# Performance work log

Measured on AMD Instinct MI355X. Metric: run time of the kernel, lower is better.

## Reference

```python
import jax, jax.numpy as jnp
import numpy as np

N = 100_000   # number of sparse points
C = 128       # channels
K3 = 27       # 3x3x3 kernel offsets


def sparse_conv(x, nbr, W, b):
    """Minkowski-style sparse conv: gather-GEMM-scatter.
    x:   [N, Cin] point features
    nbr: [N, K3] neighbor index per kernel offset; index N -> missing (zero row)
    W:   [K3, Cin, Cout], b: [Cout]
    """
    x_pad = jnp.concatenate([x, jnp.zeros((1, x.shape[1]), x.dtype)], axis=0)

    def step(acc, wk_nk):
        Wk, nk = wk_nk                      # Wk: [Cin,Cout], nk: [N]
        return acc + x_pad[nk] @ Wk, None   # gather + GEMM, accumulate

    acc0 = jnp.broadcast_to(b, (x.shape[0], W.shape[2])).astype(x.dtype)
    acc, _ = jax.lax.scan(step, acc0, (W, nbr.T))
    return acc


def setup_inputs() -> dict:
    key = jax.random.key(0)
    ks = jax.random.split(key, 12)
    Ch = C // 2

    def w(k, shape, fan_in):
        return jax.random.normal(k, shape, dtype=jnp.float32) / np.sqrt(fan_in)

    x = jax.random.normal(ks[0], (N, C), dtype=jnp.float32)
    # neighbor map; value N means "no neighbor" (maps to zero-padded row)
    nbr = jax.random.randint(ks[1], (N, K3), 0, N + 1, dtype=jnp.int32)

    return {
        "x": x,
        "nbr": nbr,
        "W00": w(ks[2], (K3, C, Ch), K3 * C),   # conv0_0: kxkxk, C -> C/2
        "b00": jnp.zeros((Ch,), jnp.float32),
        "W01": w(ks[3], (K3, Ch, Ch), K3 * Ch),  # conv0_1: kxkxk, C/2 -> C/2
        "b01": jnp.zeros((Ch,), jnp.float32),
        "W10": w(ks[4], (C, Ch), C),             # conv1_0: 1x1x1, C -> C/2
        "b10": jnp.zeros((Ch,), jnp.float32),
        "W11": w(ks[5], (K3, Ch, Ch), K3 * Ch),  # conv1_1: kxkxk, C/2 -> C/2
        "b11": jnp.zeros((Ch,), jnp.float32),
        "W12": w(ks[6], (Ch, Ch), Ch),           # conv1_2: 1x1x1, C/2 -> C/2
        "b12": jnp.zeros((Ch,), jnp.float32),
    }


def reference(x, nbr, W00, b00, W01, b01, W10, b10, W11, b11, W12, b12):
    # branch 0: conv -> relu -> conv
    h0 = jax.nn.relu(sparse_conv(x, nbr, W00, b00))
    out0 = sparse_conv(h0, nbr, W01, b01)
    # branch 1: 1x1 conv -> relu -> conv -> relu -> 1x1 conv
    h1 = jax.nn.relu(x @ W10 + b10)
    h1 = jax.nn.relu(sparse_conv(h1, nbr, W11, b11))
    out1 = h1 @ W12 + b12
    # concat channels, residual add
    return jnp.concatenate([out0, out1], axis=1) + x
```

## Files before the change

kernel.cpp:

```cpp
#include <hip/hip_runtime.h>
#include <hip/hip_bf16.h>
#include <stdint.h>

typedef __bf16 bf16x8 __attribute__((ext_vector_type(8)));
typedef float  f32x4  __attribute__((ext_vector_type(4)));

#define MFMA(A, B, C) __builtin_amdgcn_mfma_f32_16x16x32_bf16((A), (B), (C), 0, 0, 0)

static __device__ __forceinline__ unsigned short f2b(float f) {
    union { float f; unsigned int u; } v; v.f = f;
    return (unsigned short)((v.u + 0x7FFFu + ((v.u >> 16) & 1u)) >> 16);
}

__global__ __launch_bounds__(256) void convert_kernel(
    const float* __restrict__ x, unsigned short* __restrict__ xb,
    unsigned short* __restrict__ hb, int N) {
    long long i = (long long)blockIdx.x * blockDim.x + threadIdx.x;
    long long base = i * 4;
    long long nx = (long long)N * 128;
    long long total = nx + 128;
    if (base >= total) return;
    if (base < nx) {
        float4 v = *(const float4*)(x + base);
        ushort4 o;
        o.x = f2b(v.x); o.y = f2b(v.y); o.z = f2b(v.z); o.w = f2b(v.w);
        *(ushort4*)(xb + base) = o;
    } else {
        ushort4 z = make_ushort4(0, 0, 0, 0);
        *(ushort4*)(xb + base) = z;
        *(ushort4*)(hb + base) = z;
    }
}

__global__ __launch_bounds__(256) void pack_kernel(
    const float* __restrict__ W00, const float* __restrict__ W01,
    const float* __restrict__ W10, const float* __restrict__ W11,
    const float* __restrict__ W12,
    unsigned short* __restrict__ wp00, unsigned short* __restrict__ wp01,
    unsigned short* __restrict__ wp10, unsigned short* __restrict__ wp11,
    unsigned short* __restrict__ wp12) {
    int g = blockIdx.x * blockDim.x + threadIdx.x;
    const float* W; unsigned short* out; int cinSteps;
    if (g < 27648)      { W = W00; out = wp00; cinSteps = 4; }
    else if (g < 41472) { g -= 27648; W = W01; out = wp01; cinSteps = 2; }
    else if (g < 55296) { g -= 41472; W = W11; out = wp11; cinSteps = 2; }
    else if (g < 56320) { g -= 55296; W = W10; out = wp10; cinSteps = 4; }
    else if (g < 56832) { g -= 56320; W = W12; out = wp12; cinSteps = 2; }
    else return;
    int lane = g & 63;
    int st   = g >> 6;
    int t    = st & 3;
    int s    = st >> 2;
    int q = lane >> 4, n16 = lane & 15;
    int k    = s / cinSteps;
    int cinb = (s % cinSteps) * 32;
    int Cin  = cinSteps * 32;
    int cout = t * 16 + n16;
    unsigned short o[8];
#pragma unroll
    for (int j = 0; j < 8; ++j) {
        float v = W[(size_t)(k * Cin + cinb + q * 8 + j) * 64 + cout];
        o[j] = f2b(v);
    }
    *(ushort4*)(out + (size_t)g * 8)     = make_ushort4(o[0], o[1], o[2], o[3]);
    *(ushort4*)(out + (size_t)g * 8 + 4) = make_ushort4(o[4], o[5], o[6], o[7]);
}

__global__ __launch_bounds__(256, 2) void passB_kernel(
    const unsigned short* __restrict__ xb, const int* __restrict__ nbr,
    const unsigned short* __restrict__ wp00, const unsigned short* __restrict__ wp10,
    const float* __restrict__ b00, const float* __restrict__ b10,
    unsigned short* __restrict__ hb, int N) {
    int lane = threadIdx.x & 63;
    int wv   = threadIdx.x >> 6;
    int q = lane >> 4, n16 = lane & 15;
    int rowbase = blockIdx.x * 128 + wv * 32;

    f32x4 acc0[2][4];
    f32x4 acc1[2][4];
#pragma unroll
    for (int rs = 0; rs < 2; ++rs)
#pragma unroll
        for (int t = 0; t < 4; ++t) { acc0[rs][t] = (f32x4)0.f; acc1[rs][t] = (f32x4)0.f; }

    int mc0 = min(rowbase + n16, N - 1);
    int mc1 = min(rowbase + 16 + n16, N - 1);

    for (int k = 0; k < 27; ++k) {
        int r0 = nbr[(size_t)mc0 * 27 + k];
        int r1 = nbr[(size_t)mc1 * 27 + k];
        const unsigned short* a0p = xb + (size_t)r0 * 128 + q * 8;
        const unsigned short* a1p = xb + (size_t)r1 * 128 + q * 8;
#pragma unroll
        for (int s2 = 0; s2 < 4; ++s2) {
            bf16x8 A0 = *(const bf16x8*)(a0p + s2 * 32);
            bf16x8 A1 = *(const bf16x8*)(a1p + s2 * 32);
            const unsigned short* bp = wp00 + ((size_t)(k * 4 + s2) * 4 * 64) * 8 + lane * 8;
#pragma unroll
            for (int t = 0; t < 4; ++t) {
                bf16x8 B = *(const bf16x8*)(bp + t * 512);
                acc0[0][t] = MFMA(A0, B, acc0[0][t]);
                acc0[1][t] = MFMA(A1, B, acc0[1][t]);
            }
        }
    }
    {
        const unsigned short* a0p = xb + (size_t)mc0 * 128 + q * 8;
        const unsigned short* a1p = xb + (size_t)mc1 * 128 + q * 8;
#pragma unroll
        for (int s2 = 0; s2 < 4; ++s2) {
            bf16x8 A0 = *(const bf16x8*)(a0p + s2 * 32);
            bf16x8 A1 = *(const bf16x8*)(a1p + s2 * 32);
            const unsigned short* bp = wp10 + (size_t)(s2 * 4) * 64 * 8 + lane * 8;
#pragma unroll
            for (int t = 0; t < 4; ++t) {
                bf16x8 B = *(const bf16x8*)(bp + t * 512);
                acc1[0][t] = MFMA(A0, B, acc1[0][t]);
                acc1[1][t] = MFMA(A1, B, acc1[1][t]);
            }
        }
    }
#pragma unroll
    for (int rs = 0; rs < 2; ++rs)
#pragma unroll
        for (int t = 0; t < 4; ++t) {
            int col = t * 16 + n16;
            float bb0 = b00[col], bb1 = b10[col];
#pragma unroll
            for (int r = 0; r < 4; ++r) {
                int row = rowbase + rs * 16 + q * 4 + r;
                if (row < N) {
                    float h0 = fmaxf(acc0[rs][t][r] + bb0, 0.f);
                    float h1 = fmaxf(acc1[rs][t][r] + bb1, 0.f);
                    hb[(size_t)row * 128 + col]      = f2b(h0);
                    hb[(size_t)row * 128 + 64 + col] = f2b(h1);
                }
            }
        }
}

__global__ __launch_bounds__(256, 2) void passC_kernel(
    const unsigned short* __restrict__ hb, const int* __restrict__ nbr,
    const float* __restrict__ x,
    const unsigned short* __restrict__ wp01, const unsigned short* __restrict__ wp11,
    const unsigned short* __restrict__ wp12,
    const float* __restrict__ b01, const float* __restrict__ b11,
    const float* __restrict__ b12, float* __restrict__ out, int N) {
    __shared__ __align__(16) unsigned short lds[4 * 2 * 16 * 72];
    int lane = threadIdx.x & 63;
    int wv   = threadIdx.x >> 6;
    int q = lane >> 4, n16 = lane & 15;
    int rowbase = blockIdx.x * 128 + wv * 32;

    f32x4 accO0[2][4];
    f32x4 accT[2][4];
#pragma unroll
    for (int rs = 0; rs < 2; ++rs)
#pragma unroll
        for (int t = 0; t < 4; ++t) { accO0[rs][t] = (f32x4)0.f; accT[rs][t] = (f32x4)0.f; }

    int mc0 = min(rowbase + n16, N - 1);
    int mc1 = min(rowbase + 16 + n16, N - 1);

    for (int k = 0; k < 27; ++k) {
        int r0 = nbr[(size_t)mc0 * 27 + k];
        int r1 = nbr[(size_t)mc1 * 27 + k];
        const unsigned short* g0 = hb + (size_t)r0 * 128;
        const unsigned short* g1 = hb + (size_t)r1 * 128;
#pragma unroll
        for (int s2 = 0; s2 < 2; ++s2) {
            bf16x8 A0 = *(const bf16x8*)(g0 + s2 * 32 + q * 8);
            bf16x8 A1 = *(const bf16x8*)(g1 + s2 * 32 + q * 8);
            const unsigned short* bp = wp01 + ((size_t)(k * 2 + s2) * 4 * 64) * 8 + lane * 8;
#pragma unroll
            for (int t = 0; t < 4; ++t) {
                bf16x8 B = *(const bf16x8*)(bp + t * 512);
                accO0[0][t] = MFMA(A0, B, accO0[0][t]);
                accO0[1][t] = MFMA(A1, B, accO0[1][t]);
            }
            bf16x8 C0 = *(const bf16x8*)(g0 + 64 + s2 * 32 + q * 8);
            bf16x8 C1 = *(const bf16x8*)(g1 + 64 + s2 * 32 + q * 8);
            const unsigned short* bp2 = wp11 + ((size_t)(k * 2 + s2) * 4 * 64) * 8 + lane * 8;
#pragma unroll
            for (int t = 0; t < 4; ++t) {
                bf16x8 B = *(const bf16x8*)(bp2 + t * 512);
                accT[0][t] = MFMA(C0, B, accT[0][t]);
                accT[1][t] = MFMA(C1, B, accT[1][t]);
            }
        }
    }

    unsigned short* myl = lds + (size_t)wv * (2 * 16 * 72);
#pragma unroll
    for (int rs = 0; rs < 2; ++rs)
#pragma unroll
        for (int t = 0; t < 4; ++t) {
            int col = t * 16 + n16;
            float bo = b01[col], bt = b11[col];
#pragma unroll
            for (int r = 0; r < 4; ++r) {
                int row = rowbase + rs * 16 + q * 4 + r;
                if (row < N)
                    out[(size_t)row * 128 + col] =
                        accO0[rs][t][r] + bo + x[(size_t)row * 128 + col];
                float tv = fmaxf(accT[rs][t][r] + bt, 0.f);
                myl[(rs * 16 + q * 4 + r) * 72 + col] = f2b(tv);
            }
        }
    __syncthreads();

    f32x4 accO1[2][4];
#pragma unroll
    for (int rs = 0; rs < 2; ++rs)
#pragma unroll
        for (int t = 0; t < 4; ++t) accO1[rs][t] = (f32x4)0.f;
#pragma unroll
    for (int s2 = 0; s2 < 2; ++s2) {
        bf16x8 A0 = *(const bf16x8*)(myl + (0 * 16 + n16) * 72 + s2 * 32 + q * 8);
        bf16x8 A1 = *(const bf16x8*)(myl + (16 + n16) * 72 + s2 * 32 + q * 8);
        const unsigned short* bp = wp12 + (size_t)(s2 * 4) * 64 * 8 + lane * 8;
#pragma unroll
        for (int t = 0; t < 4; ++t) {
            bf16x8 B = *(const bf16x8*)(bp + t * 512);
            accO1[0][t] = MFMA(A0, B, accO1[0][t]);
            accO1[1][t] = MFMA(A1, B, accO1[1][t]);
        }
    }
#pragma unroll
    for (int rs = 0; rs < 2; ++rs)
#pragma unroll
        for (int t = 0; t < 4; ++t) {
            int col = t * 16 + n16;
            float bo = b12[col];
#pragma unroll
            for (int r = 0; r < 4; ++r) {
                int row = rowbase + rs * 16 + q * 4 + r;
                if (row < N)
                    out[(size_t)row * 128 + 64 + col] =
                        accO1[rs][t][r] + bo + x[(size_t)row * 128 + 64 + col];
            }
        }
}

extern "C" void kernel_launch(void* const* d_in, const int* in_sizes, int n_in,
                              void* d_out, int out_size, void* d_ws, size_t ws_size,
                              hipStream_t stream) {
    const float* x   = (const float*)d_in[0];
    const int*   nbr = (const int*)d_in[1];
    const float* W00 = (const float*)d_in[2];
    const float* b00 = (const float*)d_in[3];
    const float* W01 = (const float*)d_in[4];
    const float* b01 = (const float*)d_in[5];
    const float* W10 = (const float*)d_in[6];
    const float* b10 = (const float*)d_in[7];
    const float* W11 = (const float*)d_in[8];
    const float* b11 = (const float*)d_in[9];
    const float* W12 = (const float*)d_in[10];
    const float* b12 = (const float*)d_in[11];
    float* out = (float*)d_out;
    int N = in_sizes[0] / 128;

    char* ws = (char*)d_ws;
    size_t cur = 0;
    unsigned short* xb = (unsigned short*)(ws + cur); cur += (size_t)(N + 1) * 128 * 2;
    unsigned short* hb = (unsigned short*)(ws + cur); cur += (size_t)(N + 1) * 128 * 2;
    unsigned short* wp00 = (unsigned short*)(ws + cur); cur += 27648 * 8 * 2;
    unsigned short* wp01 = (unsigned short*)(ws + cur); cur += 13824 * 8 * 2;
    unsigned short* wp11 = (unsigned short*)(ws + cur); cur += 13824 * 8 * 2;
    unsigned short* wp10 = (unsigned short*)(ws + cur); cur += 1024 * 8 * 2;
    unsigned short* wp12 = (unsigned short*)(ws + cur); cur += 512 * 8 * 2;

    long long cvt_groups = ((long long)N * 128 + 128) / 4;
    int cvt_blocks = (int)((cvt_groups + 255) / 256);
    convert_kernel<<<cvt_blocks, 256, 0, stream>>>(x, xb, hb, N);
    pack_kernel<<<222, 256, 0, stream>>>(W00, W01, W10, W11, W12,
                                         wp00, wp01, wp10, wp11, wp12);
    int blocks = (N + 127) / 128;
    passB_kernel<<<blocks, 256, 0, stream>>>(xb, nbr, wp00, wp10, b00, b10, hb, N);
    passC_kernel<<<blocks, 256, 0, stream>>>(hb, nbr, x, wp01, wp11, wp12,
                                             b01, b11, b12, out, N);
}
```

Baseline: 480.6 us.

## Halve rows per wave and software-pipeline neighbor gathers in sparse conv passes

Each wave now handles 16 rows instead of 32, with 64 rows per block, twice as many blocks, and launch bounds raised to 4 blocks per CU for higher occupancy. The neighbor feature gather for offset k+1, and the index load for k+2, are prefetched into registers while the MFMAs for offset k run, to hide gather latency. In passB the last prefetched row is the center row, so the 1x1 conv reuses it instead of reloading. The trade-off is that each weight fragment loaded now feeds half as many MFMAs, so weight traffic per unit of work doubles.

```diff
diff --git a/kernel.cpp b/kernel.cpp
--- a/kernel.cpp
+++ b/kernel.cpp
@@ -66,7 +66,7 @@
     *(ushort4*)(out + (size_t)g * 8 + 4) = make_ushort4(o[4], o[5], o[6], o[7]);
 }
 
-__global__ __launch_bounds__(256, 2) void passB_kernel(
+__global__ __launch_bounds__(256, 4) void passB_kernel(
     const unsigned short* __restrict__ xb, const int* __restrict__ nbr,
     const unsigned short* __restrict__ wp00, const unsigned short* __restrict__ wp10,
     const float* __restrict__ b00, const float* __restrict__ b10,
@@ -74,172 +74,180 @@
     int lane = threadIdx.x & 63;
     int wv   = threadIdx.x >> 6;
     int q = lane >> 4, n16 = lane & 15;
-    int rowbase = blockIdx.x * 128 + wv * 32;
-
-    f32x4 acc0[2][4];
-    f32x4 acc1[2][4];
-#pragma unroll
-    for (int rs = 0; rs < 2; ++rs)
-#pragma unroll
-        for (int t = 0; t < 4; ++t) { acc0[rs][t] = (f32x4)0.f; acc1[rs][t] = (f32x4)0.f; }
-
-    int mc0 = min(rowbase + n16, N - 1);
-    int mc1 = min(rowbase + 16 + n16, N - 1);
+    int rowbase = blockIdx.x * 64 + wv * 16;
+
+    f32x4 acc0[4];
+    f32x4 acc1[4];
+#pragma unroll
+    for (int t = 0; t < 4; ++t) { acc0[t] = (f32x4)0.f; acc1[t] = (f32x4)0.f; }
+
+    int mc = min(rowbase + n16, N - 1);
+    size_t nb = (size_t)mc * 27;
+    int idx1 = nbr[nb];
+    int idx2 = nbr[nb + 1];
+
+    bf16x8 Ac[4];
+    {
+        const unsigned short* ap = xb + (size_t)idx1 * 128 + q * 8;
+#pragma unroll
+        for (int s2 = 0; s2 < 4; ++s2) Ac[s2] = *(const bf16x8*)(ap + s2 * 32);
+    }
+    idx1 = idx2;
 
     for (int k = 0; k < 27; ++k) {
-        int r0 = nbr[(size_t)mc0 * 27 + k];
-        int r1 = nbr[(size_t)mc1 * 27 + k];
-        const unsigned short* a0p = xb + (size_t)r0 * 128 + q * 8;
-        const unsigned short* a1p = xb + (size_t)r1 * 128 + q * 8;
-#pragma unroll
-        for (int s2 = 0; s2 < 4; ++s2) {
-            bf16x8 A0 = *(const bf16x8*)(a0p + s2 * 32);
-            bf16x8 A1 = *(const bf16x8*)(a1p + s2 * 32);
-            const unsigned short* bp = wp00 + ((size_t)(k * 4 + s2) * 4 * 64) * 8 + lane * 8;
-#pragma unroll
-            for (int t = 0; t < 4; ++t) {
-                bf16x8 B = *(const bf16x8*)(bp + t * 512);
-                acc0[0][t] = MFMA(A0, B, acc0[0][t]);
-                acc0[1][t] = MFMA(A1, B, acc0[1][t]);
-            }
-        }
-    }
+        int idxn = (k + 2 < 27) ? nbr[nb + k + 2] : mc;
+        bf16x8 An[4];
+        {
+            const unsigned short* ap = xb + (size_t)idx1 * 128 + q * 8;
+#pragma unroll
+            for (int s2 = 0; s2 < 4; ++s2) An[s2] = *(const bf16x8*)(ap + s2 * 32);
+        }
+        const unsigned short* bp = wp00 + (size_t)k * 8192 + lane * 8;
+#pragma unroll
+        for (int s2 = 0; s2 < 4; ++s2)
+#pragma unroll
+            for (int t = 0; t < 4; ++t) {
+                bf16x8 B = *(const bf16x8*)(bp + s2 * 2048 + t * 512);
+                acc0[t] = MFMA(Ac[s2], B, acc0[t]);
+            }
+#pragma unroll
+        for (int s2 = 0; s2 < 4; ++s2) Ac[s2] = An[s2];
+        idx1 = idxn;
+    }
+
     {
-        const unsigned short* a0p = xb + (size_t)mc0 * 128 + q * 8;
-        const unsigned short* a1p = xb + (size_t)mc1 * 128 + q * 8;
-#pragma unroll
-        for (int s2 = 0; s2 < 4; ++s2) {
-            bf16x8 A0 = *(const bf16x8*)(a0p + s2 * 32);
-            bf16x8 A1 = *(const bf16x8*)(a1p + s2 * 32);
-            const unsigned short* bp = wp10 + (size_t)(s2 * 4) * 64 * 8 + lane * 8;
-#pragma unroll
-            for (int t = 0; t < 4; ++t) {
-                bf16x8 B = *(const bf16x8*)(bp + t * 512);
-                acc1[0][t] = MFMA(A0, B, acc1[0][t]);
-                acc1[1][t] = MFMA(A1, B, acc1[1][t]);
-            }
-        }
-    }
-#pragma unroll
-    for (int rs = 0; rs < 2; ++rs)
-#pragma unroll
-        for (int t = 0; t < 4; ++t) {
-            int col = t * 16 + n16;
-            float bb0 = b00[col], bb1 = b10[col];
-#pragma unroll
-            for (int r = 0; r < 4; ++r) {
-                int row = rowbase + rs * 16 + q * 4 + r;
-                if (row < N) {
-                    float h0 = fmaxf(acc0[rs][t][r] + bb0, 0.f);
-                    float h1 = fmaxf(acc1[rs][t][r] + bb1, 0.f);
-                    hb[(size_t)row * 128 + col]      = f2b(h0);
-                    hb[(size_t)row * 128 + 64 + col] = f2b(h1);
-                }
-            }
-        }
-}
-
-__global__ __launch_bounds__(256, 2) void passC_kernel(
+        const unsigned short* bp = wp10 + lane * 8;
+#pragma unroll
+        for (int s2 = 0; s2 < 4; ++s2)
+#pragma unroll
+            for (int t = 0; t < 4; ++t) {
+                bf16x8 B = *(const bf16x8*)(bp + s2 * 2048 + t * 512);
+                acc1[t] = MFMA(Ac[s2], B, acc1[t]);
+            }
+    }
+
+#pragma unroll
+    for (int t = 0; t < 4; ++t) {
+        int col = t * 16 + n16;
+        float bb0 = b00[col], bb1 = b10[col];
+#pragma unroll
+        for (int r = 0; r < 4; ++r) {
+            int row = rowbase + q * 4 + r;
+            if (row < N) {
+                hb[(size_t)row * 128 + col]      = f2b(fmaxf(acc0[t][r] + bb0, 0.f));
+                hb[(size_t)row * 128 + 64 + col] = f2b(fmaxf(acc1[t][r] + bb1, 0.f));
+            }
+        }
+    }
+}
+
+__global__ __launch_bounds__(256, 4) void passC_kernel(
     const unsigned short* __restrict__ hb, const int* __restrict__ nbr,
     const float* __restrict__ x,
     const unsigned short* __restrict__ wp01, const unsigned short* __restrict__ wp11,
     const unsigned short* __restrict__ wp12,
     const float* __restrict__ b01, const float* __restrict__ b11,
     const float* __restrict__ b12, float* __restrict__ out, int N) {
-    __shared__ __align__(16) unsigned short lds[4 * 2 * 16 * 72];
+    __shared__ __align__(16) unsigned short lds[4 * 16 * 72];
     int lane = threadIdx.x & 63;
     int wv   = threadIdx.x >> 6;
     int q = lane >> 4, n16 = lane & 15;
-    int rowbase = blockIdx.x * 128 + wv * 32;
-
-    f32x4 accO0[2][4];
-    f32x4 accT[2][4];
-#pragma unroll
-    for (int rs = 0; rs < 2; ++rs)
-#pragma unroll
-        for (int t = 0; t < 4; ++t) { accO0[rs][t] = (f32x4)0.f; accT[rs][t] = (f32x4)0.f; }
-
-    int mc0 = min(rowbase + n16, N - 1);
-    int mc1 = min(rowbase + 16 + n16, N - 1);
+    int rowbase = blockIdx.x * 64 + wv * 16;
+
+    f32x4 accO0[4];
+    f32x4 accT[4];
+#pragma unroll
+    for (int t = 0; t < 4; ++t) { accO0[t] = (f32x4)0.f; accT[t] = (f32x4)0.f; }
+
+    int mc = min(rowbase + n16, N - 1);
+    size_t nb = (size_t)mc * 27;
+    int idx1 = nbr[nb];
+    int idx2 = nbr[nb + 1];
+
+    bf16x8 Ac[2], Cc[2];
+    {
+        const unsigned short* g = hb + (size_t)idx1 * 128 + q * 8;
+#pragma unroll
+        for (int s2 = 0; s2 < 2; ++s2) {
+            Ac[s2] = *(const bf16x8*)(g + s2 * 32);
+            Cc[s2] = *(const bf16x8*)(g + 64 + s2 * 32);
+        }
+    }
+    idx1 = idx2;
 
     for (int k = 0; k < 27; ++k) {
-        int r0 = nbr[(size_t)mc0 * 27 + k];
-        int r1 = nbr[(size_t)mc1 * 27 + k];
-        const unsigned short* g0 = hb + (size_t)r0 * 128;
-        const unsigned short* g1 = hb + (size_t)r1 * 128;
+        int idxn = (k + 2 < 27) ? nbr[nb + k + 2] : N;
+        bf16x8 An[2], Cn[2];
+        {
+            const unsigned short* g = hb + (size_t)idx1 * 128 + q * 8;
+#pragma unroll
+            for (int s2 = 0; s2 < 2; ++s2) {
+                An[s2] = *(const bf16x8*)(g + s2 * 32);
+                Cn[s2] = *(const bf16x8*)(g + 64 + s2 * 32);
+            }
+        }
 #pragma unroll
         for (int s2 = 0; s2 < 2; ++s2) {
-            bf16x8 A0 = *(const bf16x8*)(g0 + s2 * 32 + q * 8);
-            bf16x8 A1 = *(const bf16x8*)(g1 + s2 * 32 + q * 8);
-            const unsigned short* bp = wp01 + ((size_t)(k * 2 + s2) * 4 * 64) * 8 + lane * 8;
+            const unsigned short* bp  = wp01 + (size_t)(k * 2 + s2) * 2048 + lane * 8;
+            const unsigned short* bp2 = wp11 + (size_t)(k * 2 + s2) * 2048 + lane * 8;
 #pragma unroll
             for (int t = 0; t < 4; ++t) {
                 bf16x8 B = *(const bf16x8*)(bp + t * 512);
-                accO0[0][t] = MFMA(A0, B, accO0[0][t]);
-                accO0[1][t] = MFMA(A1, B, accO0[1][t]);
-            }
-            bf16x8 C0 = *(const bf16x8*)(g0 + 64 + s2 * 32 + q * 8);
-            bf16x8 C1 = *(const bf16x8*)(g1 + 64 + s2 * 32 + q * 8);
-            const unsigned short* bp2 = wp11 + ((size_t)(k * 2 + s2) * 4 * 64) * 8 + lane * 8;
-#pragma unroll
-            for (int t = 0; t < 4; ++t) {
-                bf16x8 B = *(const bf16x8*)(bp2 + t * 512);
-                accT[0][t] = MFMA(C0, B, accT[0][t]);
-                accT[1][t] = MFMA(C1, B, accT[1][t]);
-            }
-        }
-    }
-
-    unsigned short* myl = lds + (size_t)wv * (2 * 16 * 72);
-#pragma unroll
-    for (int rs = 0; rs < 2; ++rs)
-#pragma unroll
-        for (int t = 0; t < 4; ++t) {
-            int col = t * 16 + n16;
-            float bo = b01[col], bt = b11[col];
-#pragma unroll
-            for (int r = 0; r < 4; ++r) {
-                int row = rowbase + rs * 16 + q * 4 + r;
-                if (row < N)
-                    out[(size_t)row * 128 + col] =
-                        accO0[rs][t][r] + bo + x[(size_t)row * 128 + col];
-                float tv = fmaxf(accT[rs][t][r] + bt, 0.f);
-                myl[(rs * 16 + q * 4 + r) * 72 + col] = f2b(tv);
-            }
-        }
+                accO0[t] = MFMA(Ac[s2], B, accO0[t]);
+            }
+#pragma unroll
+            for (int t = 0; t < 4; ++t) {
+                bf16x8 B2 = *(const bf16x8*)(bp2 + t * 512);
+                accT[t] = MFMA(Cc[s2], B2, accT[t]);
+            }
+        }
+#pragma unroll
+        for (int s2 = 0; s2 < 2; ++s2) { Ac[s2] = An[s2]; Cc[s2] = Cn[s2]; }
+        idx1 = idxn;
+    }
+
+    unsigned short* myl = lds + (size_t)wv * (16 * 72);
+#pragma unroll
+    for (int t = 0; t < 4; ++t) {
+        int col = t * 16 + n16;
+        float bo = b01[col], bt = b11[col];
+#pragma unroll
+        for (int r = 0; r < 4; ++r) {
+            int row = rowbase + q * 4 + r;
+            if (row < N)
+                out[(size_t)row * 128 + col] =
+                    accO0[t][r] + bo + x[(size_t)row * 128 + col];
+            float tv = fmaxf(accT[t][r] + bt, 0.f);
+            myl[(q * 4 + r) * 72 + col] = f2b(tv);
+        }
+    }
     __syncthreads();
 
-    f32x4 accO1[2][4];
-#pragma unroll
-    for (int rs = 0; rs < 2; ++rs)
-#pragma unroll
-        for (int t = 0; t < 4; ++t) accO1[rs][t] = (f32x4)0.f;
+    f32x4 accO1[4];
+#pragma unroll
+    for (int t = 0; t < 4; ++t) accO1[t] = (f32x4)0.f;
 #pragma unroll
     for (int s2 = 0; s2 < 2; ++s2) {
-        bf16x8 A0 = *(const bf16x8*)(myl + (0 * 16 + n16) * 72 + s2 * 32 + q * 8);
-        bf16x8 A1 = *(const bf16x8*)(myl + (16 + n16) * 72 + s2 * 32 + q * 8);
-        const unsigned short* bp = wp12 + (size_t)(s2 * 4) * 64 * 8 + lane * 8;
+        bf16x8 A = *(const bf16x8*)(myl + n16 * 72 + s2 * 32 + q * 8);
+        const unsigned short* bp = wp12 + (size_t)s2 * 2048 + lane * 8;
 #pragma unroll
         for (int t = 0; t < 4; ++t) {
             bf16x8 B = *(const bf16x8*)(bp + t * 512);
-            accO1[0][t] = MFMA(A0, B, accO1[0][t]);
-            accO1[1][t] = MFMA(A1, B, accO1[1][t]);
-        }
-    }
-#pragma unroll
-    for (int rs = 0; rs < 2; ++rs)
-#pragma unroll
-        for (int t = 0; t < 4; ++t) {
-            int col = t * 16 + n16;
-            float bo = b12[col];
-#pragma unroll
-            for (int r = 0; r < 4; ++r) {
-                int row = rowbase + rs * 16 + q * 4 + r;
-                if (row < N)
-                    out[(size_t)row * 128 + 64 + col] =
-                        accO1[rs][t][r] + bo + x[(size_t)row * 128 + 64 + col];
-            }
-        }
+            accO1[t] = MFMA(A, B, accO1[t]);
+        }
+    }
+#pragma unroll
+    for (int t = 0; t < 4; ++t) {
+        int col = t * 16 + n16;
+        float bo = b12[col];
+#pragma unroll
+        for (int r = 0; r < 4; ++r) {
+            int row = rowbase + q * 4 + r;
+            if (row < N)
+                out[(size_t)row * 128 + 64 + col] =
+                    accO1[t][r] + bo + x[(size_t)row * 128 + 64 + col];
+        }
+    }
 }
 
 extern "C" void kernel_launch(void* const* d_in, const int* in_sizes, int n_in,
@@ -275,7 +283,7 @@
     convert_kernel<<<cvt_blocks, 256, 0, stream>>>(x, xb, hb, N);
     pack_kernel<<<222, 256, 0, stream>>>(W00, W01, W10, W11, W12,
                                          wp00, wp01, wp10, wp11, wp12);
-    int blocks = (N + 127) / 128;
+    int blocks = (N + 63) / 64;
     passB_kernel<<<blocks, 256, 0, stream>>>(xb, nbr, wp00, wp10, b00, b10, hb, N);
     passC_kernel<<<blocks, 256, 0, stream>>>(hb, nbr, x, wp01, wp11, wp12,
                                              b01, b11, b12, out, N);
```

New measurement: 533.0 us. +10.9%, slower.

## Stage per-offset weights in double-buffered LDS and prefetch next neighbor gathers

Applied to the files above, without the earlier changes.

Both gather-GEMM passes now cooperatively load each kernel offset's weight slice into a double-buffered shared-memory tile. They also register-prefetch the next offset's gathered rows and neighbor indices, so global loads overlap the MFMA work. PassC's two weight sets are interleaved per offset into one packed buffer so each stage is loaded in one contiguous transfer. PassB reuses the final centre-row registers for the 1x1 conv. PassC uses nontemporal loads and stores for the residual and output. This adds a block-wide barrier per offset and about 32KB of LDS per block, which may limit occupancy.

```diff
diff --git a/kernel.cpp b/kernel.cpp
--- a/kernel.cpp
+++ b/kernel.cpp
@@ -36,16 +36,15 @@
     const float* __restrict__ W00, const float* __restrict__ W01,
     const float* __restrict__ W10, const float* __restrict__ W11,
     const float* __restrict__ W12,
-    unsigned short* __restrict__ wp00, unsigned short* __restrict__ wp01,
-    unsigned short* __restrict__ wp10, unsigned short* __restrict__ wp11,
-    unsigned short* __restrict__ wp12) {
+    unsigned short* __restrict__ wp00, unsigned short* __restrict__ wpC,
+    unsigned short* __restrict__ wp10, unsigned short* __restrict__ wp12) {
     int g = blockIdx.x * blockDim.x + threadIdx.x;
-    const float* W; unsigned short* out; int cinSteps;
-    if (g < 27648)      { W = W00; out = wp00; cinSteps = 4; }
-    else if (g < 41472) { g -= 27648; W = W01; out = wp01; cinSteps = 2; }
-    else if (g < 55296) { g -= 41472; W = W11; out = wp11; cinSteps = 2; }
-    else if (g < 56320) { g -= 55296; W = W10; out = wp10; cinSteps = 4; }
-    else if (g < 56832) { g -= 56320; W = W12; out = wp12; cinSteps = 2; }
+    const float* W; int cinSteps; int which;
+    if (g < 27648)      { W = W00; cinSteps = 4; which = 0; }
+    else if (g < 41472) { g -= 27648; W = W01; cinSteps = 2; which = 1; }
+    else if (g < 55296) { g -= 41472; W = W11; cinSteps = 2; which = 2; }
+    else if (g < 56320) { g -= 55296; W = W10; cinSteps = 4; which = 3; }
+    else if (g < 56832) { g -= 56320; W = W12; cinSteps = 2; which = 4; }
     else return;
     int lane = g & 63;
     int st   = g >> 6;
@@ -62,8 +61,16 @@
         float v = W[(size_t)(k * Cin + cinb + q * 8 + j) * 64 + cout];
         o[j] = f2b(v);
     }
-    *(ushort4*)(out + (size_t)g * 8)     = make_ushort4(o[0], o[1], o[2], o[3]);
-    *(ushort4*)(out + (size_t)g * 8 + 4) = make_ushort4(o[4], o[5], o[6], o[7]);
+    unsigned short* dst;
+    if (which == 0)      dst = wp00 + (size_t)g * 8;
+    else if (which == 1) dst = wpC + (size_t)k * 8192 +
+                               ((size_t)(((s & 1) * 4 + t) * 64 + lane)) * 8;
+    else if (which == 2) dst = wpC + (size_t)k * 8192 + 4096 +
+                               ((size_t)(((s & 1) * 4 + t) * 64 + lane)) * 8;
+    else if (which == 3) dst = wp10 + (size_t)g * 8;
+    else                 dst = wp12 + (size_t)g * 8;
+    *(ushort4*)(dst)     = make_ushort4(o[0], o[1], o[2], o[3]);
+    *(ushort4*)(dst + 4) = make_ushort4(o[4], o[5], o[6], o[7]);
 }
 
 __global__ __launch_bounds__(256, 2) void passB_kernel(
@@ -71,8 +78,10 @@
     const unsigned short* __restrict__ wp00, const unsigned short* __restrict__ wp10,
     const float* __restrict__ b00, const float* __restrict__ b10,
     unsigned short* __restrict__ hb, int N) {
-    int lane = threadIdx.x & 63;
-    int wv   = threadIdx.x >> 6;
+    __shared__ __align__(16) unsigned short bbuf[2][8192];
+    int tid = threadIdx.x;
+    int lane = tid & 63;
+    int wv   = tid >> 6;
     int q = lane >> 4, n16 = lane & 15;
     int rowbase = blockIdx.x * 128 + wv * 32;
 
@@ -85,41 +94,75 @@
 
     int mc0 = min(rowbase + n16, N - 1);
     int mc1 = min(rowbase + 16 + n16, N - 1);
+    size_t nb0 = (size_t)mc0 * 27, nb1 = (size_t)mc1 * 27;
+
+    int ia = nbr[nb0], ib = nbr[nb1];
+    int4 br[4];
+#pragma unroll
+    for (int j = 0; j < 4; ++j) br[j] = *(const int4*)(wp00 + j * 2048 + tid * 8);
+    bf16x8 A0c[4], A1c[4];
+    {
+        const unsigned short* p0 = xb + (size_t)ia * 128 + q * 8;
+        const unsigned short* p1 = xb + (size_t)ib * 128 + q * 8;
+#pragma unroll
+        for (int s2 = 0; s2 < 4; ++s2) {
+            A0c[s2] = *(const bf16x8*)(p0 + s2 * 32);
+            A1c[s2] = *(const bf16x8*)(p1 + s2 * 32);
+        }
+    }
+    int ian = nbr[nb0 + 1], ibn = nbr[nb1 + 1];
+#pragma unroll
+    for (int j = 0; j < 4; ++j) *(int4*)(&bbuf[0][j * 2048 + tid * 8]) = br[j];
+    __syncthreads();
 
     for (int k = 0; k < 27; ++k) {
-        int r0 = nbr[(size_t)mc0 * 27 + k];
-        int r1 = nbr[(size_t)mc1 * 27 + k];
-        const unsigned short* a0p = xb + (size_t)r0 * 128 + q * 8;
-        const unsigned short* a1p = xb + (size_t)r1 * 128 + q * 8;
-#pragma unroll
-        for (int s2 = 0; s2 < 4; ++s2) {
-            bf16x8 A0 = *(const bf16x8*)(a0p + s2 * 32);
-            bf16x8 A1 = *(const bf16x8*)(a1p + s2 * 32);
-            const unsigned short* bp = wp00 + ((size_t)(k * 4 + s2) * 4 * 64) * 8 + lane * 8;
+        int buf = k & 1;
+        if (k < 26) {
+            const unsigned short* src = wp00 + (size_t)(k + 1) * 8192;
+#pragma unroll
+            for (int j = 0; j < 4; ++j) br[j] = *(const int4*)(src + j * 2048 + tid * 8);
+        }
+        int ia2 = (k + 2 < 27) ? nbr[nb0 + k + 2] : mc0;
+        int ib2 = (k + 2 < 27) ? nbr[nb1 + k + 2] : mc1;
+        bf16x8 A0n[4], A1n[4];
+        {
+            const unsigned short* p0 = xb + (size_t)ian * 128 + q * 8;
+            const unsigned short* p1 = xb + (size_t)ibn * 128 + q * 8;
+#pragma unroll
+            for (int s2 = 0; s2 < 4; ++s2) {
+                A0n[s2] = *(const bf16x8*)(p0 + s2 * 32);
+                A1n[s2] = *(const bf16x8*)(p1 + s2 * 32);
+            }
+        }
+        const unsigned short* lb = &bbuf[buf][0];
+#pragma unroll
+        for (int s2 = 0; s2 < 4; ++s2)
 #pragma unroll
             for (int t = 0; t < 4; ++t) {
-                bf16x8 B = *(const bf16x8*)(bp + t * 512);
-                acc0[0][t] = MFMA(A0, B, acc0[0][t]);
-                acc0[1][t] = MFMA(A1, B, acc0[1][t]);
-            }
-        }
-    }
-    {
-        const unsigned short* a0p = xb + (size_t)mc0 * 128 + q * 8;
-        const unsigned short* a1p = xb + (size_t)mc1 * 128 + q * 8;
-#pragma unroll
-        for (int s2 = 0; s2 < 4; ++s2) {
-            bf16x8 A0 = *(const bf16x8*)(a0p + s2 * 32);
-            bf16x8 A1 = *(const bf16x8*)(a1p + s2 * 32);
-            const unsigned short* bp = wp10 + (size_t)(s2 * 4) * 64 * 8 + lane * 8;
-#pragma unroll
-            for (int t = 0; t < 4; ++t) {
-                bf16x8 B = *(const bf16x8*)(bp + t * 512);
-                acc1[0][t] = MFMA(A0, B, acc1[0][t]);
-                acc1[1][t] = MFMA(A1, B, acc1[1][t]);
-            }
-        }
-    }
+                bf16x8 B = *(const bf16x8*)(lb + (s2 * 4 + t) * 512 + lane * 8);
+                acc0[0][t] = MFMA(A0c[s2], B, acc0[0][t]);
+                acc0[1][t] = MFMA(A1c[s2], B, acc0[1][t]);
+            }
+        if (k < 26) {
+#pragma unroll
+            for (int j = 0; j < 4; ++j)
+                *(int4*)(&bbuf[buf ^ 1][j * 2048 + tid * 8]) = br[j];
+        }
+#pragma unroll
+        for (int s2 = 0; s2 < 4; ++s2) { A0c[s2] = A0n[s2]; A1c[s2] = A1n[s2]; }
+        ian = ia2; ibn = ib2;
+        __syncthreads();
+    }
+
+#pragma unroll
+    for (int s2 = 0; s2 < 4; ++s2)
+#pragma unroll
+        for (int t = 0; t < 4; ++t) {
+            bf16x8 B = *(const bf16x8*)(wp10 + s2 * 2048 + t * 512 + lane * 8);
+            acc1[0][t] = MFMA(A0c[s2], B, acc1[0][t]);
+            acc1[1][t] = MFMA(A1c[s2], B, acc1[1][t]);
+        }
+
 #pragma unroll
     for (int rs = 0; rs < 2; ++rs)
 #pragma unroll
@@ -130,10 +173,8 @@
             for (int r = 0; r < 4; ++r) {
                 int row = rowbase + rs * 16 + q * 4 + r;
                 if (row < N) {
-                    float h0 = fmaxf(acc0[rs][t][r] + bb0, 0.f);
-                    float h1 = fmaxf(acc1[rs][t][r] + bb1, 0.f);
-                    hb[(size_t)row * 128 + col]      = f2b(h0);
-                    hb[(size_t)row * 128 + 64 + col] = f2b(h1);
+                    hb[(size_t)row * 128 + col]      = f2b(fmaxf(acc0[rs][t][r] + bb0, 0.f));
+                    hb[(size_t)row * 128 + 64 + col] = f2b(fmaxf(acc1[rs][t][r] + bb1, 0.f));
                 }
             }
         }
@@ -142,13 +183,13 @@
 __global__ __launch_bounds__(256, 2) void passC_kernel(
     const unsigned short* __restrict__ hb, const int* __restrict__ nbr,
     const float* __restrict__ x,
-    const unsigned short* __restrict__ wp01, const unsigned short* __restrict__ wp11,
-    const unsigned short* __restrict__ wp12,
+    const unsigned short* __restrict__ wpC, const unsigned short* __restrict__ wp12,
     const float* __restrict__ b01, const float* __restrict__ b11,
     const float* __restrict__ b12, float* __restrict__ out, int N) {
-    __shared__ __align__(16) unsigned short lds[4 * 2 * 16 * 72];
-    int lane = threadIdx.x & 63;
-    int wv   = threadIdx.x >> 6;
+    __shared__ __align__(16) unsigned short bbuf[2][8192];
+    int tid = threadIdx.x;
+    int lane = tid & 63;
+    int wv   = tid >> 6;
     int q = lane >> 4, n16 = lane & 15;
     int rowbase = blockIdx.x * 128 + wv * 32;
 
@@ -161,36 +202,82 @@
 
     int mc0 = min(rowbase + n16, N - 1);
     int mc1 = min(rowbase + 16 + n16, N - 1);
+    size_t nb0 = (size_t)mc0 * 27, nb1 = (size_t)mc1 * 27;
+
+    int ia = nbr[nb0], ib = nbr[nb1];
+    int4 br[4];
+#pragma unroll
+    for (int j = 0; j < 4; ++j) br[j] = *(const int4*)(wpC + j * 2048 + tid * 8);
+    bf16x8 A0c[2], C0c[2], A1c[2], C1c[2];
+    {
+        const unsigned short* p0 = hb + (size_t)ia * 128 + q * 8;
+        const unsigned short* p1 = hb + (size_t)ib * 128 + q * 8;
+#pragma unroll
+        for (int s2 = 0; s2 < 2; ++s2) {
+            A0c[s2] = *(const bf16x8*)(p0 + s2 * 32);
+            C0c[s2] = *(const bf16x8*)(p0 + 64 + s2 * 32);
+            A1c[s2] = *(const bf16x8*)(p1 + s2 * 32);
+            C1c[s2] = *(const bf16x8*)(p1 + 64 + s2 * 32);
+        }
+    }
+    int ian = nbr[nb0 + 1], ibn = nbr[nb1 + 1];
+#pragma unroll
+    for (int j = 0; j < 4; ++j) *(int4*)(&bbuf[0][j * 2048 + tid * 8]) = br[j];
+    __syncthreads();
 
     for (int k = 0; k < 27; ++k) {
-        int r0 = nbr[(size_t)mc0 * 27 + k];
-        int r1 = nbr[(size_t)mc1 * 27 + k];
-        const unsigned short* g0 = hb + (size_t)r0 * 128;
-        const unsigned short* g1 = hb + (size_t)r1 * 128;
+        int buf = k & 1;
+        if (k < 26) {
+            const unsigned short* src = wpC + (size_t)(k + 1) * 8192;
+#pragma unroll
+            for (int j = 0; j < 4; ++j) br[j] = *(const int4*)(src + j * 2048 + tid * 8);
+        }
+        int ia2 = (k + 2 < 27) ? nbr[nb0 + k + 2] : N;
+        int ib2 = (k + 2 < 27) ? nbr[nb1 + k + 2] : N;
+        bf16x8 A0n[2], C0n[2], A1n[2], C1n[2];
+        {
+            const unsigned short* p0 = hb + (size_t)ian * 128 + q * 8;
+            const unsigned short* p1 = hb + (size_t)ibn * 128 + q * 8;
+#pragma unroll
+            for (int s2 = 0; s2 < 2; ++s2) {
+                A0n[s2] = *(const bf16x8*)(p0 + s2 * 32);
+                C0n[s2] = *(const bf16x8*)(p0 + 64 + s2 * 32);
+                A1n[s2] = *(const bf16x8*)(p1 + s2 * 32);
+                C1n[s2] = *(const bf16x8*)(p1 + 64 + s2 * 32);
+            }
+        }
+        const unsigned short* lb = &bbuf[buf][0];
 #pragma unroll
         for (int s2 = 0; s2 < 2; ++s2) {
-            bf16x8 A0 = *(const bf16x8*)(g0 + s2 * 32 + q * 8);
-            bf16x8 A1 = *(const bf16x8*)(g1 + s2 * 32 + q * 8);
-            const unsigned short* bp = wp01 + ((size_t)(k * 2 + s2) * 4 * 64) * 8 + lane * 8;
 #pragma unroll
             for (int t = 0; t < 4; ++t) {
-                bf16x8 B = *(const bf16x8*)(bp + t * 512);
-                accO0[0][t] = MFMA(A0, B, accO0[0][t]);
-                accO0[1][t] = MFMA(A1, B, accO0[1][t]);
-            }
-            bf16x8 C0 = *(const bf16x8*)(g0 + 64 + s2 * 32 + q * 8);
-            bf16x8 C1 = *(const bf16x8*)(g1 + 64 + s2 * 32 + q * 8);
-            const unsigned short* bp2 = wp11 + ((size_t)(k * 2 + s2) * 4 * 64) * 8 + lane * 8;
+                bf16x8 B = *(const bf16x8*)(lb + (s2 * 4 + t) * 512 + lane * 8);
+                accO0[0][t] = MFMA(A0c[s2], B, accO0[0][t]);
+                accO0[1][t] = MFMA(A1c[s2], B, accO0[1][t]);
+            }
 #pragma unroll
             for (int t = 0; t < 4; ++t) {
-                bf16x8 B = *(const bf16x8*)(bp2 + t * 512);
-                accT[0][t] = MFMA(C0, B, accT[0][t]);
-                accT[1][t] = MFMA(C1, B, accT[1][t]);
-            }
-        }
-    }
-
-    unsigned short* myl = lds + (size_t)wv * (2 * 16 * 72);
+                bf16x8 B2 = *(const bf16x8*)(lb + 4096 + (s2 * 4 + t) * 512 + lane * 8);
+                accT[0][t] = MFMA(C0c[s2], B2, accT[0][t]);
+                accT[1][t] = MFMA(C1c[s2], B2, accT[1][t]);
+            }
+        }
+        if (k < 26) {
+#pragma unroll
+            for (int j = 0; j < 4; ++j)
+                *(int4*)(&bbuf[buf ^ 1][j * 2048 + tid * 8]) = br[j];
+        }
+#pragma unroll
+        for (int s2 = 0; s2 < 2; ++s2) {
+            A0c[s2] = A0n[s2]; C0c[s2] = C0n[s2];
+            A1c[s2] = A1n[s2]; C1c[s2] = C1n[s2];
+        }
+        ian = ia2; ibn = ib2;
+        __syncthreads();
+    }
+
+    unsigned short* scratch = &bbuf[0][0];
+    unsigned short* myl = scratch + wv * 2304;
 #pragma unroll
     for (int rs = 0; rs < 2; ++rs)
 #pragma unroll
@@ -200,14 +287,15 @@
 #pragma unroll
             for (int r = 0; r < 4; ++r) {
                 int row = rowbase + rs * 16 + q * 4 + r;
-                if (row < N)
-                    out[(size_t)row * 128 + col] =
-                        accO0[rs][t][r] + bo + x[(size_t)row * 128 + col];
+                if (row < N) {
+                    float xv = __builtin_nontemporal_load(x + (size_t)row * 128 + col);
+                    __builtin_nontemporal_store(accO0[rs][t][r] + bo + xv,
+                                                out + (size_t)row * 128 + col);
+                }
                 float tv = fmaxf(accT[rs][t][r] + bt, 0.f);
                 myl[(rs * 16 + q * 4 + r) * 72 + col] = f2b(tv);
             }
         }
-    __syncthreads();
 
     f32x4 accO1[2][4];
 #pragma unroll
@@ -216,12 +304,11 @@
         for (int t = 0; t < 4; ++t) accO1[rs][t] = (f32x4)0.f;
 #pragma unroll
     for (int s2 = 0; s2 < 2; ++s2) {
-        bf16x8 A0 = *(const bf16x8*)(myl + (0 * 16 + n16) * 72 + s2 * 32 + q * 8);
+        bf16x8 A0 = *(const bf16x8*)(myl + n16 * 72 + s2 * 32 + q * 8);
         bf16x8 A1 = *(const bf16x8*)(myl + (16 + n16) * 72 + s2 * 32 + q * 8);
-        const unsigned short* bp = wp12 + (size_t)(s2 * 4) * 64 * 8 + lane * 8;
-#pragma unroll
-        for (int t = 0; t < 4; ++t) {
-            bf16x8 B = *(const bf16x8*)(bp + t * 512);
+#pragma unroll
+        for (int t = 0; t < 4; ++t) {
+            bf16x8 B = *(const bf16x8*)(wp12 + s2 * 2048 + t * 512 + lane * 8);
             accO1[0][t] = MFMA(A0, B, accO1[0][t]);
             accO1[1][t] = MFMA(A1, B, accO1[1][t]);
         }
@@ -235,9 +322,11 @@
 #pragma unroll
             for (int r = 0; r < 4; ++r) {
                 int row = rowbase + rs * 16 + q * 4 + r;
-                if (row < N)
-                    out[(size_t)row * 128 + 64 + col] =
-                        accO1[rs][t][r] + bo + x[(size_t)row * 128 + 64 + col];
+                if (row < N) {
+                    float xv = __builtin_nontemporal_load(x + (size_t)row * 128 + 64 + col);
+                    __builtin_nontemporal_store(accO1[rs][t][r] + bo + xv,
+                                                out + (size_t)row * 128 + 64 + col);
+                }
             }
         }
 }
@@ -262,21 +351,20 @@
 
     char* ws = (char*)d_ws;
     size_t cur = 0;
-    unsigned short* xb = (unsigned short*)(ws + cur); cur += (size_t)(N + 1) * 128 * 2;
-    unsigned short* hb = (unsigned short*)(ws + cur); cur += (size_t)(N + 1) * 128 * 2;
+    unsigned short* xb  = (unsigned short*)(ws + cur); cur += (size_t)(N + 1) * 128 * 2;
+    unsigned short* hb  = (unsigned short*)(ws + cur); cur += (size_t)(N + 1) * 128 * 2;
     unsigned short* wp00 = (unsigned short*)(ws + cur); cur += 27648 * 8 * 2;
-    unsigned short* wp01 = (unsigned short*)(ws + cur); cur += 13824 * 8 * 2;
-    unsigned short* wp11 = (unsigned short*)(ws + cur); cur += 13824 * 8 * 2;
-    unsigned short* wp10 = (unsigned short*)(ws + cur); cur += 1024 * 8 * 2;
-    unsigned short* wp12 = (unsigned short*)(ws + cur); cur += 512 * 8 * 2;
+    unsigned short* wpC  = (unsigned short*)(ws + cur); cur += (size_t)27 * 8192 * 2;
+    unsigned short* wp10 = (unsigned short*)(ws + cur); cur += 8192 * 2;
+    unsigned short* wp12 = (unsigned short*)(ws + cur); cur += 4096 * 2;
 
     long long cvt_groups = ((long long)N * 128 + 128) / 4;
     int cvt_blocks = (int)((cvt_groups + 255) / 256);
     convert_kernel<<<cvt_blocks, 256, 0, stream>>>(x, xb, hb, N);
     pack_kernel<<<222, 256, 0, stream>>>(W00, W01, W10, W11, W12,
-                                         wp00, wp01, wp10, wp11, wp12);
+                                         wp00, wpC, wp10, wp12);
     int blocks = (N + 127) / 128;
     passB_kernel<<<blocks, 256, 0, stream>>>(xb, nbr, wp00, wp10, b00, b10, hb, N);
-    passC_kernel<<<blocks, 256, 0, stream>>>(hb, nbr, x, wp01, wp11, wp12,
+    passC_kernel<<<blocks, 256, 0, stream>>>(hb, nbr, x, wpC, wp12,
                                              b01, b11, b12, out, N);
 }
```

Measured after the change: 437.8 us. 8.9% less time.
